# Kernel tuning notes

Measured on AMD Instinct MI355X. Metric: run time of the kernel, lower is better.

Reference implementation:

```python
import jax, jax.numpy as jnp
import numpy as np

SHIFTS = [1, 3, 5, 7]
C = 16  # in_channels // 4
# -1 neighbor offsets for tmp1..tmp8 (dy, dx) in units of the dilation
OFFSETS = [(-1, -1), (-1, 0), (-1, 1), (0, 1), (1, 1), (1, 0), (1, -1), (0, -1)]


def setup_inputs() -> dict:
    key = jax.random.key(0)
    ks = jax.random.split(key, 32)
    d = {}
    d['cen'] = jax.random.normal(ks[0], (8, 64, 256, 256), jnp.float32)
    d['mas'] = jax.random.normal(ks[1], (8, 1, 256, 256), jnp.float32)
    d['in_conv_w'] = jax.random.normal(ks[2], (16, 64), jnp.float32) * 0.1
    d['in_conv_b'] = jax.random.normal(ks[3], (16,), jnp.float32) * 0.1
    for i, s in enumerate(SHIFTS):
        d[f'dw_w{s}'] = jax.random.normal(ks[4 + 2 * i], (16, 1, s, s), jnp.float32) * 0.1
        d[f'dw_b{s}'] = jax.random.normal(ks[5 + 2 * i], (16,), jnp.float32) * 0.1
    d['l1_w'] = jax.random.normal(ks[12], (4, 16, 4), jnp.float32) * 0.1
    d['l1_b'] = jax.random.normal(ks[13], (4, 16), jnp.float32) * 0.1
    d['l2_w'] = jax.random.normal(ks[14], (4, 16, 8), jnp.float32) * 0.1
    d['l2_b'] = jax.random.normal(ks[15], (4, 16), jnp.float32) * 0.1
    d['base_w'] = jax.random.normal(ks[16], (16, 4), jnp.float32) * 0.1
    d['bn_scale'] = jnp.ones((16,), jnp.float32)
    d['bn_bias'] = jnp.zeros((16,), jnp.float32)
    d['final_w'] = jax.random.normal(ks[17], (1, 16), jnp.float32) * 0.1
    d['final_b'] = jax.random.normal(ks[18], (1,), jnp.float32) * 0.1
    return d


def _dw_conv(x, w, b, pad):
    # depthwise conv, groups == channels
    y = jax.lax.conv_general_dilated(
        x, w, window_strides=(1, 1), padding=[(pad, pad), (pad, pad)],
        dimension_numbers=('NCHW', 'OIHW', 'NCHW'), feature_group_count=x.shape[1])
    return y + b[None, :, None, None]


def _shifted(x, dy, dx, d):
    # zero-padded shift: out(y,x) = in(y+dy, x+dx)
    H, W = x.shape[2], x.shape[3]
    p = jnp.pad(x, ((0, 0), (0, 0), (d, d), (d, d)))
    return p[:, :, d + dy:d + dy + H, d + dx:d + dx + W]


def _circ_shift(x, dw_w, dw_b, w1, b1, w2, b2, shift):
    x = _dw_conv(x, dw_w, dw_b, shift // 2)
    # tmp_k = x - x shifted by the k-th neighbor offset (dilation = shift)
    T = [x - _shifted(x, dy * shift, dx * shift, shift) for dy, dx in OFFSETS]
    # paired sums: S[k] = tmp_{k+1} + tmp_{k+5} (S repeats with period 4)
    S = [T[k] + T[k + 4] for k in range(4)]
    outs = []
    for k in range(8):  # fixed small structural loop
        feats = jnp.stack([S[(k + 1) % 4], S[(k + 3) % 4], S[(k + 2) % 4],
                           2.0 * T[(k + 4) % 8]], axis=2)  # (B,C,4,H,W)
        # grouped 1x1 conv (groups=C, 4C->C) == per-channel contraction over feature axis
        o = jnp.einsum('bcfhw,cf->bchw', feats, w1) + b1[None, :, None, None]
        outs.append(o * T[k])
    O = jnp.sort(jnp.stack(outs, axis=2), axis=2)  # (B,C,8,H,W) sorted over branch axis
    return jnp.einsum('bcfhw,cf->bchw', O, w2) + b2[None, :, None, None]


def reference(cen, mas, in_conv_w, in_conv_b, dw_w1, dw_b1, dw_w3, dw_b3,
              dw_w5, dw_b5, dw_w7, dw_b7, l1_w, l1_b, l2_w, l2_b,
              base_w, bn_scale, bn_bias, final_w, final_b):
    # in_conv: 1x1, in_channels -> C
    x = jnp.einsum('bihw,oi->bohw', cen, in_conv_w) + in_conv_b[None, :, None, None]
    dws = [(dw_w1, dw_b1), (dw_w3, dw_b3), (dw_w5, dw_b5), (dw_w7, dw_b7)]
    branches = [
        _circ_shift(x, dws[i][0], dws[i][1], l1_w[i], l1_b[i], l2_w[i], l2_b[i], SHIFTS[i])
        for i in range(len(SHIFTS))
    ]
    A = jnp.sort(jnp.stack(branches, axis=2), axis=2)  # (B,C,4,H,W)
    # out_conv: grouped 1x1 BaseConv (conv no-bias + BN(affine) + SiLU), then 1x1 -> 1, sigmoid
    y = jnp.einsum('bcfhw,cf->bchw', A, base_w)
    y = jax.nn.silu(y * bn_scale[None, :, None, None] + bn_bias[None, :, None, None])
    y = jnp.einsum('bchw,oc->bohw', y, final_w) + final_b[None, :, None, None]
    return jax.nn.sigmoid(y)
```

## Files before the change

kernel.cpp:

```cpp
#include <hip/hip_runtime.h>
#include <hip/hip_fp16.h>
#include <math.h>

#define HW 65536

typedef float v2f __attribute__((ext_vector_type(2), aligned(4)));
typedef _Float16 h2 __attribute__((ext_vector_type(2)));

__global__ __launch_bounds__(256, 8) void k_inconv(const float* __restrict__ cen,
                                                   const float* __restrict__ w,
                                                   const float* __restrict__ bias,
                                                   float* __restrict__ x) {
    int px = blockIdx.x * 256 + threadIdx.x;
    int b  = px >> 16;
    int hw = px & 65535;

    const float* src = cen + (long)(b * 64) * HW + hw;
    float acc[16];
#pragma unroll
    for (int o = 0; o < 16; o++) acc[o] = bias[o];

#pragma unroll 4
    for (int i = 0; i < 64; i++) {
        float v = src[(long)i * HW];
#pragma unroll
        for (int o = 0; o < 16; o++) acc[o] = fmaf(v, w[o * 64 + i], acc[o]);
    }
    float* dst = x + (long)(b * 16) * HW + hw;
#pragma unroll
    for (int o = 0; o < 16; o++) dst[(long)o * HW] = acc[o];
}

#define CEH(a, b) { h2 _t = __builtin_elementwise_min(a, b); \
                    b = __builtin_elementwise_max(a, b); a = _t; }

__device__ __forceinline__ void sort8_h2(h2* v) {
    CEH(v[0], v[1]); CEH(v[2], v[3]); CEH(v[4], v[5]); CEH(v[6], v[7]);
    CEH(v[0], v[2]); CEH(v[1], v[3]); CEH(v[4], v[6]); CEH(v[5], v[7]);
    CEH(v[1], v[2]); CEH(v[5], v[6]); CEH(v[0], v[4]); CEH(v[3], v[7]);
    CEH(v[1], v[5]); CEH(v[2], v[6]);
    CEH(v[1], v[4]); CEH(v[3], v[6]);
    CEH(v[2], v[4]); CEH(v[3], v[5]);
    CEH(v[3], v[4]);
}
__device__ __forceinline__ void sort4_h2(h2* v) {
    CEH(v[0], v[1]); CEH(v[2], v[3]); CEH(v[0], v[2]); CEH(v[1], v[3]); CEH(v[1], v[2]);
}

#define LXS 56
#define SS  48

__global__ __launch_bounds__(512, 4) void k_main(
    const float* __restrict__ x,
    const float* __restrict__ dw_w1, const float* __restrict__ dw_b1,
    const float* __restrict__ dw_w3, const float* __restrict__ dw_b3,
    const float* __restrict__ dw_w5, const float* __restrict__ dw_b5,
    const float* __restrict__ dw_w7, const float* __restrict__ dw_b7,
    const float* __restrict__ l1w, const float* __restrict__ l1b,
    const float* __restrict__ l2w, const float* __restrict__ l2b,
    const float* __restrict__ bw,  const float* __restrict__ bns,
    const float* __restrict__ bnb, __half* __restrict__ y16) {

    const int plane = blockIdx.y;
    const int c     = plane & 15;
    const int ty0   = (blockIdx.x >> 3) * 32;
    const int tx0   = (blockIdx.x & 7) * 32;
    const int tid   = threadIdx.x;

    __shared__ float lx[52 * LXS];
    __shared__ float lxs[4][46 * SS];

    const float* xp = x + (long)plane * HW;

    for (int i = tid; i < 52 * 52; i += 512) {
        int r  = i / 52;
        int cc = i - r * 52;
        int gy = ty0 - 10 + r, gx = tx0 - 10 + cc;
        float v = 0.f;
        if ((unsigned)gy < 256u && (unsigned)gx < 256u) v = xp[gy * 256 + gx];
        lx[r * LXS + cc] = v;
    }
    __syncthreads();

    const float* W7 = dw_w7 + c * 49;
    const float* W5 = dw_w5 + c * 25;
    const float* W3 = dw_w3 + c * 9;
    const float  W1 = dw_w1[c];
    const float  B1 = dw_b1[c], B3 = dw_b3[c], B5 = dw_b5[c], B7 = dw_b7[c];

    for (int u = tid; u < 46 * 23; u += 512) {
        int row = u / 23;
        int pc0 = (u - row * 23) * 2;
        v2f c7 = {0, 0}, c5 = {0, 0}, c3 = {0, 0}, c1 = {0, 0};
#pragma unroll
        for (int a = 0; a < 7; a++) {
            const float* rp = &lx[(row + a) * LXS + pc0];
            v2f q0 = *(const v2f*)rp;
            v2f q1 = *(const v2f*)(rp + 2);
            v2f q2 = *(const v2f*)(rp + 4);
            v2f q3 = *(const v2f*)(rp + 6);
            float v8 = rp[8];
            float v[9] = {q0.x, q0.y, q1.x, q1.y, q2.x, q2.y, q3.x, q3.y, v8};
#pragma unroll
            for (int bb = 0; bb < 7; bb++) {
                v2f vv = {v[bb], v[bb + 1]};
                c7 += vv * W7[a * 7 + bb];
            }
            if (a >= 1 && a <= 5) {
#pragma unroll
                for (int bb = 0; bb < 5; bb++) {
                    v2f vv = {v[bb + 1], v[bb + 2]};
                    c5 += vv * W5[(a - 1) * 5 + bb];
                }
            }
            if (a >= 2 && a <= 4) {
#pragma unroll
                for (int bb = 0; bb < 3; bb++) {
                    v2f vv = {v[bb + 2], v[bb + 3]};
                    c3 += vv * W3[(a - 2) * 3 + bb];
                }
            }
            if (a == 3) {
                v2f vv = {v[3], v[4]};
                c1 = vv * W1;
            }
        }
        int gy  = ty0 - 7 + row;
        int gx0 = tx0 - 7 + pc0;
        bool rin = ((unsigned)gy < 256u);
        bool in0 = rin && ((unsigned)gx0 < 256u);
        bool in1 = rin && ((unsigned)(gx0 + 1) < 256u);
        int o = row * SS + pc0;
        v2f s;
        s.x = in0 ? c1.x + B1 : 0.f; s.y = in1 ? c1.y + B1 : 0.f;
        *(v2f*)&lxs[0][o] = s;
        s.x = in0 ? c3.x + B3 : 0.f; s.y = in1 ? c3.y + B3 : 0.f;
        *(v2f*)&lxs[1][o] = s;
        s.x = in0 ? c5.x + B5 : 0.f; s.y = in1 ? c5.y + B5 : 0.f;
        *(v2f*)&lxs[2][o] = s;
        s.x = in0 ? c7.x + B7 : 0.f; s.y = in1 ? c7.y + B7 : 0.f;
        *(v2f*)&lxs[3][o] = s;
    }
    __syncthreads();

    const int ty  = tid >> 4;
    const int tx2 = (tid & 15) * 2;
    const int gy  = ty0 + ty, gx = tx0 + tx2;
    const int corner = ty * SS + tx2;

    v2f br[4];
#pragma unroll
    for (int i = 0; i < 4; i++) {
        const int s = 1 + 2 * i;
        const float* xs = lxs[i];
        v2f ctr = *(const v2f*)&xs[corner + 7 * SS + 7];
        v2f n0  = *(const v2f*)&xs[corner + (7 - s) * SS + (7 - s)];
        v2f n1  = *(const v2f*)&xs[corner + (7 - s) * SS + 7];
        v2f n2  = *(const v2f*)&xs[corner + (7 - s) * SS + (7 + s)];
        v2f n3  = *(const v2f*)&xs[corner + 7 * SS + (7 + s)];
        v2f n4  = *(const v2f*)&xs[corner + (7 + s) * SS + (7 + s)];
        v2f n5  = *(const v2f*)&xs[corner + (7 + s) * SS + 7];
        v2f n6  = *(const v2f*)&xs[corner + (7 + s) * SS + (7 - s)];
        v2f n7  = *(const v2f*)&xs[corner + 7 * SS + (7 - s)];

        v2f T[8];
        T[0] = ctr - n0; T[1] = ctr - n1; T[2] = ctr - n2; T[3] = ctr - n3;
        T[4] = ctr - n4; T[5] = ctr - n5; T[6] = ctr - n6; T[7] = ctr - n7;
        v2f S[4];
#pragma unroll
        for (int k = 0; k < 4; k++) S[k] = T[k] + T[k + 4];

        const float w10   = l1w[i * 64 + c * 4 + 0];
        const float w11   = l1w[i * 64 + c * 4 + 1];
        const float w12   = l1w[i * 64 + c * 4 + 2];
        const float w13x2 = 2.f * l1w[i * 64 + c * 4 + 3];
        const float bb1   = l1b[i * 16 + c];

        v2f R[4];
#pragma unroll
        for (int m = 0; m < 4; m++) {
            v2f r = S[(m + 2) & 3] * w12 + bb1;
            r = S[(m + 3) & 3] * w11 + r;
            r = S[(m + 1) & 3] * w10 + r;
            R[m] = r;
        }

        h2 h8[8];
#pragma unroll
        for (int k = 0; k < 8; k++) {
            v2f o = (T[(k + 4) & 7] * w13x2 + R[k & 3]) * T[k];
            h8[k] = __builtin_convertvector(o, h2);
        }
        sort8_h2(h8);

        v2f acc = {l2b[i * 16 + c], l2b[i * 16 + c]};
#pragma unroll
        for (int k = 0; k < 8; k++) {
            v2f ov = __builtin_convertvector(h8[k], v2f);
            acc += ov * l2w[i * 128 + c * 8 + k];
        }
        br[i] = acc;
    }

    h2 bh[4];
#pragma unroll
    for (int i = 0; i < 4; i++) bh[i] = __builtin_convertvector(br[i], h2);
    sort4_h2(bh);

    v2f yv = {0.f, 0.f};
#pragma unroll
    for (int i = 0; i < 4; i++) {
        v2f bv = __builtin_convertvector(bh[i], v2f);
        yv += bv * bw[c * 4 + i];
    }
    const float bsc = bns[c], bbi = bnb[c];
    float zx = fmaf(yv.x, bsc, bbi);
    float zy = fmaf(yv.y, bsc, bbi);
    float sx = zx / (1.f + __expf(-zx));
    float sy = zy / (1.f + __expf(-zy));
    *(__half2*)&y16[(long)plane * HW + gy * 256 + gx] = __floats2half2_rn(sx, sy);
}

__global__ __launch_bounds__(256) void k_final(const __half* __restrict__ y16,
                                               const float* __restrict__ fw,
                                               const float* __restrict__ fb,
                                               float* __restrict__ out) {
    long t  = (long)blockIdx.x * 256 + threadIdx.x;
    long p0 = t * 2;
    int  b  = (int)(p0 >> 16);
    int  hw = (int)(p0 & 65535);

    float accx = fb[0], accy = fb[0];
#pragma unroll
    for (int cc = 0; cc < 16; cc++) {
        __half2 h = *(const __half2*)(y16 + (long)(b * 16 + cc) * HW + hw);
        float2 v = __half22float2(h);
        float wv = fw[cc];
        accx = fmaf(v.x, wv, accx);
        accy = fmaf(v.y, wv, accy);
    }
    float2 r;
    r.x = 1.f / (1.f + __expf(-accx));
    r.y = 1.f / (1.f + __expf(-accy));
    *(float2*)(out + p0) = r;
}

extern "C" void kernel_launch(void* const* d_in, const int* in_sizes, int n_in,
                              void* d_out, int out_size, void* d_ws, size_t ws_size,
                              hipStream_t stream) {
    (void)in_sizes; (void)n_in; (void)out_size; (void)ws_size;
    const float* cen   = (const float*)d_in[0];
    const float* in_w  = (const float*)d_in[2];
    const float* in_b  = (const float*)d_in[3];
    const float* dw_w1 = (const float*)d_in[4];
    const float* dw_b1 = (const float*)d_in[5];
    const float* dw_w3 = (const float*)d_in[6];
    const float* dw_b3 = (const float*)d_in[7];
    const float* dw_w5 = (const float*)d_in[8];
    const float* dw_b5 = (const float*)d_in[9];
    const float* dw_w7 = (const float*)d_in[10];
    const float* dw_b7 = (const float*)d_in[11];
    const float* l1w   = (const float*)d_in[12];
    const float* l1b   = (const float*)d_in[13];
    const float* l2w   = (const float*)d_in[14];
    const float* l2b   = (const float*)d_in[15];
    const float* bw    = (const float*)d_in[16];
    const float* bns   = (const float*)d_in[17];
    const float* bnb   = (const float*)d_in[18];
    const float* fw    = (const float*)d_in[19];
    const float* fb    = (const float*)d_in[20];

    float*  xbuf = (float*)d_ws;
    __half* y16  = (__half*)(xbuf + (size_t)8 * 16 * HW);
    float*  out  = (float*)d_out;

    k_inconv<<<2048, 256, 0, stream>>>(cen, in_w, in_b, xbuf);
    k_main<<<dim3(64, 128), 512, 0, stream>>>(xbuf, dw_w1, dw_b1, dw_w3, dw_b3,
                                              dw_w5, dw_b5, dw_w7, dw_b7,
                                              l1w, l1b, l2w, l2b, bw, bns, bnb, y16);
    k_final<<<1024, 256, 0, stream>>>(y16, fw, fb, out);
}
```

Baseline: 393.1 us.

## Split depthwise conv into padded fp16 buffer and fuse branch math with final conv

The fused k_main is split in two. k_dw writes all four depthwise-conv outputs as fp16 into padded 272-pitch planes in global memory. k_mach reads the shifted neighbors straight from global memory, runs the circular-shift, sort and linear stages in packed half2 arithmetic with a pre-packed half weight table, and folds the final 1x1 conv and sigmoid into the same loop over channels. k_inconv now processes two pixels per thread, keeps its weights in LDS and writes fp16, and k_final is removed. This drops the redundant halo computation of the shared-memory tiles and the separate final pass. In exchange it adds a large intermediate global buffer, unaligned neighbor loads, and lower precision in the branch math.

```diff
diff --git a/kernel.cpp b/kernel.cpp
--- a/kernel.cpp
+++ b/kernel.cpp
@@ -3,32 +3,19 @@
 #include <math.h>
 
 #define HW 65536
-
-typedef float v2f __attribute__((ext_vector_type(2), aligned(4)));
+#define PITCH 272
+#define PLANE (PITCH * PITCH)
+
+typedef float v2f __attribute__((ext_vector_type(2), aligned(8)));
 typedef _Float16 h2 __attribute__((ext_vector_type(2)));
 
-__global__ __launch_bounds__(256, 8) void k_inconv(const float* __restrict__ cen,
-                                                   const float* __restrict__ w,
-                                                   const float* __restrict__ bias,
-                                                   float* __restrict__ x) {
-    int px = blockIdx.x * 256 + threadIdx.x;
-    int b  = px >> 16;
-    int hw = px & 65535;
-
-    const float* src = cen + (long)(b * 64) * HW + hw;
-    float acc[16];
-#pragma unroll
-    for (int o = 0; o < 16; o++) acc[o] = bias[o];
-
-#pragma unroll 4
-    for (int i = 0; i < 64; i++) {
-        float v = src[(long)i * HW];
-#pragma unroll
-        for (int o = 0; o < 16; o++) acc[o] = fmaf(v, w[o * 64 + i], acc[o]);
-    }
-    float* dst = x + (long)(b * 16) * HW + hw;
-#pragma unroll
-    for (int o = 0; o < 16; o++) dst[(long)o * HW] = acc[o];
+__device__ __forceinline__ h2 uh(unsigned u) { return __builtin_bit_cast(h2, u); }
+__device__ __forceinline__ h2 lda(const ushort* p) { return *(const h2*)(const void*)p; }
+__device__ __forceinline__ h2 ldu(const ushort* p) {
+    unsigned lo = *(const unsigned*)(const void*)(p - 1);
+    unsigned hi = *(const unsigned*)(const void*)(p + 1);
+    unsigned r = (hi << 16) | (lo >> 16);
+    return __builtin_bit_cast(h2, r);
 }
 
 #define CEH(a, b) { h2 _t = __builtin_elementwise_min(a, b); \
@@ -47,38 +34,88 @@
     CEH(v[0], v[1]); CEH(v[2], v[3]); CEH(v[0], v[2]); CEH(v[1], v[3]); CEH(v[1], v[2]);
 }
 
-#define LXS 56
-#define SS  48
-
-__global__ __launch_bounds__(512, 4) void k_main(
-    const float* __restrict__ x,
+__global__ __launch_bounds__(256) void k_pack(const float* __restrict__ l1w,
+                                              const float* __restrict__ l1b,
+                                              const float* __restrict__ l2w,
+                                              const float* __restrict__ l2b,
+                                              const float* __restrict__ bw,
+                                              unsigned* __restrict__ wtab) {
+    for (int t = threadIdx.x; t < 1088; t += 256) {
+        float v = 0.f;
+        if (t < 1024) {
+            int c = t >> 6, i = (t >> 4) & 3, j = t & 15;
+            if (j < 3)        v = l1w[i * 64 + c * 4 + j];
+            else if (j == 3)  v = 2.f * l1w[i * 64 + c * 4 + 3];
+            else if (j == 4)  v = l1b[i * 16 + c];
+            else if (j < 13)  v = l2w[i * 128 + c * 8 + (j - 5)];
+            else if (j == 13) v = l2b[i * 16 + c];
+        } else {
+            v = bw[t - 1024];
+        }
+        unsigned hs = (unsigned)__half_as_ushort(__float2half(v));
+        wtab[t] = hs * 0x10001u;
+    }
+}
+
+__global__ __launch_bounds__(256) void k_inconv(const float* __restrict__ cen,
+                                                const float* __restrict__ w,
+                                                const float* __restrict__ bias,
+                                                __half* __restrict__ xh) {
+    __shared__ float wl[1040];
+    int tid = threadIdx.x;
+    for (int t = tid; t < 1024; t += 256) wl[t] = w[(t & 15) * 64 + (t >> 4)];
+    if (tid < 16) wl[1024 + tid] = bias[tid];
+    __syncthreads();
+
+    int pr = blockIdx.x * 256 + tid;
+    int b_ = pr >> 15;
+    int hw = (pr & 32767) * 2;
+    const float* src = cen + (size_t)(b_ * 64) * HW + hw;
+
+    v2f acc[16];
+#pragma unroll
+    for (int o = 0; o < 16; o++) { float bv = wl[1024 + o]; v2f t = {bv, bv}; acc[o] = t; }
+
+#pragma unroll 4
+    for (int i = 0; i < 64; i++) {
+        v2f xv = *(const v2f*)(src + (size_t)i * HW);
+        const float4* wq = (const float4*)&wl[i * 16];
+#pragma unroll
+        for (int g = 0; g < 4; g++) {
+            float4 f = wq[g];
+            acc[g * 4 + 0] += xv * f.x;
+            acc[g * 4 + 1] += xv * f.y;
+            acc[g * 4 + 2] += xv * f.z;
+            acc[g * 4 + 3] += xv * f.w;
+        }
+    }
+    __half* dst = xh + (size_t)(b_ * 16) * HW + hw;
+#pragma unroll
+    for (int o = 0; o < 16; o++)
+        *(__half2*)(dst + (size_t)o * HW) = __floats2half2_rn(acc[o].x, acc[o].y);
+}
+
+__global__ __launch_bounds__(256) void k_dw(const __half* __restrict__ xh,
     const float* __restrict__ dw_w1, const float* __restrict__ dw_b1,
     const float* __restrict__ dw_w3, const float* __restrict__ dw_b3,
     const float* __restrict__ dw_w5, const float* __restrict__ dw_b5,
     const float* __restrict__ dw_w7, const float* __restrict__ dw_b7,
-    const float* __restrict__ l1w, const float* __restrict__ l1b,
-    const float* __restrict__ l2w, const float* __restrict__ l2b,
-    const float* __restrict__ bw,  const float* __restrict__ bns,
-    const float* __restrict__ bnb, __half* __restrict__ y16) {
-
+    __half* __restrict__ conv) {
     const int plane = blockIdx.y;
     const int c     = plane & 15;
-    const int ty0   = (blockIdx.x >> 3) * 32;
-    const int tx0   = (blockIdx.x & 7) * 32;
+    const int P0    = (blockIdx.x >> 2) * 68;
+    const int Q0    = (blockIdx.x & 3) * 68;
     const int tid   = threadIdx.x;
 
-    __shared__ float lx[52 * LXS];
-    __shared__ float lxs[4][46 * SS];
-
-    const float* xp = x + (long)plane * HW;
-
-    for (int i = tid; i < 52 * 52; i += 512) {
-        int r  = i / 52;
-        int cc = i - r * 52;
-        int gy = ty0 - 10 + r, gx = tx0 - 10 + cc;
+    __shared__ float lx[74 * 76];
+    const __half* xp = xh + (size_t)plane * HW;
+
+    for (int t = tid; t < 74 * 74; t += 256) {
+        int r = t / 74, cc = t - r * 74;
+        int gy = P0 - 10 + r, gx = Q0 - 10 + cc;
         float v = 0.f;
-        if ((unsigned)gy < 256u && (unsigned)gx < 256u) v = xp[gy * 256 + gx];
-        lx[r * LXS + cc] = v;
+        if ((unsigned)gy < 256u && (unsigned)gx < 256u) v = __half2float(xp[gy * 256 + gx]);
+        lx[r * 76 + cc] = v;
     }
     __syncthreads();
 
@@ -88,13 +125,13 @@
     const float  W1 = dw_w1[c];
     const float  B1 = dw_b1[c], B3 = dw_b3[c], B5 = dw_b5[c], B7 = dw_b7[c];
 
-    for (int u = tid; u < 46 * 23; u += 512) {
-        int row = u / 23;
-        int pc0 = (u - row * 23) * 2;
-        v2f c7 = {0, 0}, c5 = {0, 0}, c3 = {0, 0}, c1 = {0, 0};
+    for (int u = tid; u < 68 * 34; u += 256) {
+        int row = u / 34;
+        int pc0 = (u - row * 34) * 2;
+        v2f c7v = {0, 0}, c5v = {0, 0}, c3v = {0, 0}, c1v = {0, 0};
 #pragma unroll
         for (int a = 0; a < 7; a++) {
-            const float* rp = &lx[(row + a) * LXS + pc0];
+            const float* rp = &lx[(row + a) * 76 + pc0];
             v2f q0 = *(const v2f*)rp;
             v2f q1 = *(const v2f*)(rp + 2);
             v2f q2 = *(const v2f*)(rp + 4);
@@ -104,145 +141,118 @@
 #pragma unroll
             for (int bb = 0; bb < 7; bb++) {
                 v2f vv = {v[bb], v[bb + 1]};
-                c7 += vv * W7[a * 7 + bb];
+                c7v += vv * W7[a * 7 + bb];
             }
             if (a >= 1 && a <= 5) {
 #pragma unroll
                 for (int bb = 0; bb < 5; bb++) {
                     v2f vv = {v[bb + 1], v[bb + 2]};
-                    c5 += vv * W5[(a - 1) * 5 + bb];
+                    c5v += vv * W5[(a - 1) * 5 + bb];
                 }
             }
             if (a >= 2 && a <= 4) {
 #pragma unroll
                 for (int bb = 0; bb < 3; bb++) {
                     v2f vv = {v[bb + 2], v[bb + 3]};
-                    c3 += vv * W3[(a - 2) * 3 + bb];
+                    c3v += vv * W3[(a - 2) * 3 + bb];
                 }
             }
             if (a == 3) {
                 v2f vv = {v[3], v[4]};
-                c1 = vv * W1;
-            }
-        }
-        int gy  = ty0 - 7 + row;
-        int gx0 = tx0 - 7 + pc0;
-        bool rin = ((unsigned)gy < 256u);
-        bool in0 = rin && ((unsigned)gx0 < 256u);
-        bool in1 = rin && ((unsigned)(gx0 + 1) < 256u);
-        int o = row * SS + pc0;
-        v2f s;
-        s.x = in0 ? c1.x + B1 : 0.f; s.y = in1 ? c1.y + B1 : 0.f;
-        *(v2f*)&lxs[0][o] = s;
-        s.x = in0 ? c3.x + B3 : 0.f; s.y = in1 ? c3.y + B3 : 0.f;
-        *(v2f*)&lxs[1][o] = s;
-        s.x = in0 ? c5.x + B5 : 0.f; s.y = in1 ? c5.y + B5 : 0.f;
-        *(v2f*)&lxs[2][o] = s;
-        s.x = in0 ? c7.x + B7 : 0.f; s.y = in1 ? c7.y + B7 : 0.f;
-        *(v2f*)&lxs[3][o] = s;
-    }
-    __syncthreads();
-
-    const int ty  = tid >> 4;
-    const int tx2 = (tid & 15) * 2;
-    const int gy  = ty0 + ty, gx = tx0 + tx2;
-    const int corner = ty * SS + tx2;
-
-    v2f br[4];
-#pragma unroll
-    for (int i = 0; i < 4; i++) {
-        const int s = 1 + 2 * i;
-        const float* xs = lxs[i];
-        v2f ctr = *(const v2f*)&xs[corner + 7 * SS + 7];
-        v2f n0  = *(const v2f*)&xs[corner + (7 - s) * SS + (7 - s)];
-        v2f n1  = *(const v2f*)&xs[corner + (7 - s) * SS + 7];
-        v2f n2  = *(const v2f*)&xs[corner + (7 - s) * SS + (7 + s)];
-        v2f n3  = *(const v2f*)&xs[corner + 7 * SS + (7 + s)];
-        v2f n4  = *(const v2f*)&xs[corner + (7 + s) * SS + (7 + s)];
-        v2f n5  = *(const v2f*)&xs[corner + (7 + s) * SS + 7];
-        v2f n6  = *(const v2f*)&xs[corner + (7 + s) * SS + (7 - s)];
-        v2f n7  = *(const v2f*)&xs[corner + 7 * SS + (7 - s)];
-
-        v2f T[8];
-        T[0] = ctr - n0; T[1] = ctr - n1; T[2] = ctr - n2; T[3] = ctr - n3;
-        T[4] = ctr - n4; T[5] = ctr - n5; T[6] = ctr - n6; T[7] = ctr - n7;
-        v2f S[4];
-#pragma unroll
-        for (int k = 0; k < 4; k++) S[k] = T[k] + T[k + 4];
-
-        const float w10   = l1w[i * 64 + c * 4 + 0];
-        const float w11   = l1w[i * 64 + c * 4 + 1];
-        const float w12   = l1w[i * 64 + c * 4 + 2];
-        const float w13x2 = 2.f * l1w[i * 64 + c * 4 + 3];
-        const float bb1   = l1b[i * 16 + c];
-
-        v2f R[4];
-#pragma unroll
-        for (int m = 0; m < 4; m++) {
-            v2f r = S[(m + 2) & 3] * w12 + bb1;
-            r = S[(m + 3) & 3] * w11 + r;
-            r = S[(m + 1) & 3] * w10 + r;
-            R[m] = r;
-        }
-
-        h2 h8[8];
-#pragma unroll
-        for (int k = 0; k < 8; k++) {
-            v2f o = (T[(k + 4) & 7] * w13x2 + R[k & 3]) * T[k];
-            h8[k] = __builtin_convertvector(o, h2);
-        }
-        sort8_h2(h8);
-
-        v2f acc = {l2b[i * 16 + c], l2b[i * 16 + c]};
-#pragma unroll
-        for (int k = 0; k < 8; k++) {
-            v2f ov = __builtin_convertvector(h8[k], v2f);
-            acc += ov * l2w[i * 128 + c * 8 + k];
-        }
-        br[i] = acc;
-    }
-
-    h2 bh[4];
-#pragma unroll
-    for (int i = 0; i < 4; i++) bh[i] = __builtin_convertvector(br[i], h2);
-    sort4_h2(bh);
-
-    v2f yv = {0.f, 0.f};
-#pragma unroll
-    for (int i = 0; i < 4; i++) {
-        v2f bv = __builtin_convertvector(bh[i], v2f);
-        yv += bv * bw[c * 4 + i];
-    }
-    const float bsc = bns[c], bbi = bnb[c];
-    float zx = fmaf(yv.x, bsc, bbi);
-    float zy = fmaf(yv.y, bsc, bbi);
-    float sx = zx / (1.f + __expf(-zx));
-    float sy = zy / (1.f + __expf(-zy));
-    *(__half2*)&y16[(long)plane * HW + gy * 256 + gx] = __floats2half2_rn(sx, sy);
-}
-
-__global__ __launch_bounds__(256) void k_final(const __half* __restrict__ y16,
-                                               const float* __restrict__ fw,
-                                               const float* __restrict__ fb,
-                                               float* __restrict__ out) {
-    long t  = (long)blockIdx.x * 256 + threadIdx.x;
-    long p0 = t * 2;
-    int  b  = (int)(p0 >> 16);
-    int  hw = (int)(p0 & 65535);
-
-    float accx = fb[0], accy = fb[0];
-#pragma unroll
-    for (int cc = 0; cc < 16; cc++) {
-        __half2 h = *(const __half2*)(y16 + (long)(b * 16 + cc) * HW + hw);
-        float2 v = __half22float2(h);
-        float wv = fw[cc];
-        accx = fmaf(v.x, wv, accx);
-        accy = fmaf(v.y, wv, accy);
+                c1v = vv * W1;
+            }
+        }
+        int py = P0 + row, px = Q0 + pc0;
+        int iy = py - 7, ix = px - 7;
+        bool rin = (unsigned)iy < 256u;
+        bool in0 = rin && (unsigned)ix < 256u;
+        bool in1 = rin && (unsigned)(ix + 1) < 256u;
+        size_t o = (size_t)(plane * 4) * PLANE + (size_t)py * PITCH + px;
+        *(__half2*)&conv[o]              = __floats2half2_rn(in0 ? c1v.x + B1 : 0.f, in1 ? c1v.y + B1 : 0.f);
+        *(__half2*)&conv[o + PLANE]      = __floats2half2_rn(in0 ? c3v.x + B3 : 0.f, in1 ? c3v.y + B3 : 0.f);
+        *(__half2*)&conv[o + 2 * PLANE]  = __floats2half2_rn(in0 ? c5v.x + B5 : 0.f, in1 ? c5v.y + B5 : 0.f);
+        *(__half2*)&conv[o + 3 * PLANE]  = __floats2half2_rn(in0 ? c7v.x + B7 : 0.f, in1 ? c7v.y + B7 : 0.f);
+    }
+}
+
+__global__ __launch_bounds__(256) void k_mach(const __half* __restrict__ conv,
+                                              const unsigned* __restrict__ wtab,
+                                              const float* __restrict__ bns,
+                                              const float* __restrict__ bnb,
+                                              const float* __restrict__ fw,
+                                              const float* __restrict__ fb,
+                                              float* __restrict__ out) {
+    const int b_ = blockIdx.y;
+    const int pr = blockIdx.x * 256 + threadIdx.x;
+    const int gy = pr >> 7, gx = (pr & 127) * 2;
+    const int e0 = (gy + 7) * PITCH + (gx + 7);
+    const ushort* cb = (const ushort*)conv + (size_t)(b_ * 64) * PLANE + e0;
+
+    float fyx = fb[0], fyy = fb[0];
+
+    for (int c = 0; c < 16; c++) {
+        const ushort* cvp = cb + (size_t)(c * 4) * PLANE;
+        h2 bh[4];
+#pragma unroll
+        for (int i = 0; i < 4; i++) {
+            const int s = 1 + 2 * i;
+            const ushort* pb = cvp + (size_t)i * PLANE;
+            h2 ctr = ldu(pb);
+            h2 n0 = lda(pb - s * PITCH - s);
+            h2 n1 = ldu(pb - s * PITCH);
+            h2 n2 = lda(pb - s * PITCH + s);
+            h2 n3 = lda(pb + s);
+            h2 n4 = lda(pb + s * PITCH + s);
+            h2 n5 = ldu(pb + s * PITCH);
+            h2 n6 = lda(pb + s * PITCH - s);
+            h2 n7 = lda(pb - s);
+
+            h2 T[8];
+            T[0] = ctr - n0; T[1] = ctr - n1; T[2] = ctr - n2; T[3] = ctr - n3;
+            T[4] = ctr - n4; T[5] = ctr - n5; T[6] = ctr - n6; T[7] = ctr - n7;
+            h2 S[4];
+#pragma unroll
+            for (int k = 0; k < 4; k++) S[k] = T[k] + T[k + 4];
+
+            const unsigned* wt = wtab + ((c << 2) + i) * 16;
+            h2 w10 = uh(wt[0]), w11 = uh(wt[1]), w12 = uh(wt[2]);
+            h2 w13x2 = uh(wt[3]), bb1 = uh(wt[4]);
+
+            h2 R[4];
+#pragma unroll
+            for (int m = 0; m < 4; m++) {
+                h2 r = S[(m + 2) & 3] * w12 + bb1;
+                r = S[(m + 3) & 3] * w11 + r;
+                r = S[(m + 1) & 3] * w10 + r;
+                R[m] = r;
+            }
+            h2 h8[8];
+#pragma unroll
+            for (int k = 0; k < 8; k++)
+                h8[k] = (T[(k + 4) & 7] * w13x2 + R[k & 3]) * T[k];
+            sort8_h2(h8);
+
+            h2 acc = uh(wt[13]);
+#pragma unroll
+            for (int k = 0; k < 8; k++) acc += h8[k] * uh(wt[5 + k]);
+            bh[i] = acc;
+        }
+        sort4_h2(bh);
+        h2 yv = bh[0] * uh(wtab[1024 + (c << 2)]);
+#pragma unroll
+        for (int k = 1; k < 4; k++) yv = bh[k] * uh(wtab[1024 + (c << 2) + k]) + yv;
+
+        float zx = fmaf((float)yv.x, bns[c], bnb[c]);
+        float zy = fmaf((float)yv.y, bns[c], bnb[c]);
+        float sx = zx / (1.f + __expf(-zx));
+        float sy = zy / (1.f + __expf(-zy));
+        fyx = fmaf(sx, fw[c], fyx);
+        fyy = fmaf(sy, fw[c], fyy);
     }
     float2 r;
-    r.x = 1.f / (1.f + __expf(-accx));
-    r.y = 1.f / (1.f + __expf(-accy));
-    *(float2*)(out + p0) = r;
+    r.x = 1.f / (1.f + __expf(-fyx));
+    r.y = 1.f / (1.f + __expf(-fyy));
+    *(float2*)&out[((long)b_ << 16) + pr * 2] = r;
 }
 
 extern "C" void kernel_launch(void* const* d_in, const int* in_sizes, int n_in,
@@ -270,13 +280,14 @@
     const float* fw    = (const float*)d_in[19];
     const float* fb    = (const float*)d_in[20];
 
-    float*  xbuf = (float*)d_ws;
-    __half* y16  = (__half*)(xbuf + (size_t)8 * 16 * HW);
-    float*  out  = (float*)d_out;
-
-    k_inconv<<<2048, 256, 0, stream>>>(cen, in_w, in_b, xbuf);
-    k_main<<<dim3(64, 128), 512, 0, stream>>>(xbuf, dw_w1, dw_b1, dw_w3, dw_b3,
-                                              dw_w5, dw_b5, dw_w7, dw_b7,
-                                              l1w, l1b, l2w, l2b, bw, bns, bnb, y16);
-    k_final<<<1024, 256, 0, stream>>>(y16, fw, fb, out);
-}
+    __half*   xh   = (__half*)d_ws;
+    __half*   conv = (__half*)((char*)d_ws + (size_t)16777216);
+    unsigned* wtab = (unsigned*)((char*)d_ws + (size_t)16777216 + (size_t)75759616);
+    float*    out  = (float*)d_out;
+
+    k_pack<<<1, 256, 0, stream>>>(l1w, l1b, l2w, l2b, bw, wtab);
+    k_inconv<<<1024, 256, 0, stream>>>(cen, in_w, in_b, xh);
+    k_dw<<<dim3(16, 128), 256, 0, stream>>>(xh, dw_w1, dw_b1, dw_w3, dw_b3,
+                                            dw_w5, dw_b5, dw_w7, dw_b7, conv);
+    k_mach<<<dim3(128, 8), 256, 0, stream>>>(conv, wtab, bns, bnb, fw, fb, out);
+}
```

New measurement: 348.4 us. 11.4% less time.
